# Kernel optimization log

Measured on AMD Instinct MI355X. Metric: run time of the kernel, lower is better.

Reference implementation:

```python
import jax, jax.numpy as jnp
import numpy as np

SAMPLE_RATE = 32000.0
NUM_APPLICATIONS = 3


def _eq_biquad(x, freq, gain, q, sr):
    """torchaudio.functional.equalizer_biquad: peaking EQ biquad + lfilter.
    x: [B, T] float; freq/gain/q: scalars.
    """
    w0 = 2.0 * jnp.pi * freq / sr
    A = jnp.exp(gain / 40.0 * jnp.log(10.0))  # 10 ** (gain / 40)
    alpha = jnp.sin(w0) / (2.0 * q)
    b0 = 1.0 + alpha * A
    b1 = -2.0 * jnp.cos(w0)
    b2 = 1.0 - alpha * A
    a0 = 1.0 + alpha / A
    a1 = -2.0 * jnp.cos(w0)
    a2 = 1.0 - alpha / A
    # normalize by a0 (as torchaudio biquad -> lfilter does)
    b0, b1, b2 = b0 / a0, b1 / a0, b2 / a0
    a1, a2 = a1 / a0, a2 / a0

    B = x.shape[0]
    z = jnp.zeros((B,), x.dtype)

    def step(carry, xn):
        x1, x2, y1, y2 = carry
        yn = b0 * xn + b1 * x1 + b2 * x2 - a1 * y1 - a2 * y2
        return (xn, x1, yn, y1), yn

    # scan over time axis; carry is per-batch state vectors
    _, y = jax.lax.scan(step, (z, z, z, z), x.T)  # y: [T, B]
    return y.T


def setup_inputs() -> dict:
    key = jax.random.key(0)
    k1, k2, k3, k4 = jax.random.split(key, 4)
    clip = jax.random.normal(k1, (128, 160000), dtype=jnp.float32)
    # draws within the module's f/g/q ranges
    freqs = jax.random.uniform(k2, (NUM_APPLICATIONS,), jnp.float32, 100.0, 6000.0)
    gains = jax.random.uniform(k3, (NUM_APPLICATIONS,), jnp.float32, -8.0, 8.0)
    qs = jax.random.uniform(k4, (NUM_APPLICATIONS,), jnp.float32, 1.0, 9.0)
    return {"clip": clip, "freqs": freqs, "gains": gains, "qs": qs}


def reference(clip, freqs, gains, qs):
    x = clip
    for i in range(NUM_APPLICATIONS):
        x = _eq_biquad(x, freqs[i], gains[i], qs[i], SAMPLE_RATE)
    return x
```

## Files before the change

kernel.cpp:

```cpp
#include <hip/hip_runtime.h>
#include <math.h>

#define SRATE 32000.f
#define NB 128
#define NT 160000
#define CL 100
#define NCROW 1600
#define SEG 25
#define RECROW (NCROW*8)
#define NCHUNK (NB*NCROW)
#define NBLK (NCHUNK/64)

#ifndef M_PI
#define M_PI 3.14159265358979323846
#endif

__device__ __forceinline__ void coeffs_f32(
    const float* fr, const float* gn, const float* qs, float* c)
{
  #pragma unroll
  for (int f = 0; f < 3; ++f) {
    float w0 = 2.f * (float)M_PI * fr[f] / SRATE;
    float A  = expf(gn[f] * (2.302585093f / 40.f));
    float al = sinf(w0) / (2.f * qs[f]);
    float cw = cosf(w0);
    float a0 = 1.f + al / A;
    c[f*5+0] = (1.f + al*A) / a0;
    c[f*5+1] = -2.f * cw / a0;
    c[f*5+2] = (1.f - al*A) / a0;
    c[f*5+3] = -2.f * cw / a0;
    c[f*5+4] = (1.f - al/A) / a0;
  }
}

#define STEPR(xn, res) do { \
    float y1 = c[0]*(xn) + c[1]*x1  + c[2]*x2   - c[3]*y1p  - c[4]*y1pp;  \
    float y2 = c[5]*y1  + c[6]*y1p + c[7]*y1pp - c[8]*y2p  - c[9]*y2pp;   \
    float y3 = c[10]*y2 + c[11]*y2p + c[12]*y2pp - c[13]*y3p - c[14]*y3pp;\
    (res) = y3;                                                            \
    x2 = x1; x1 = (xn);                                                    \
    y1pp=y1p; y1p=y1; y2pp=y2p; y2p=y2; y3pp=y3p; y3p=y3;                  \
  } while (0)

#define LDG5(S, base) \
  S##0 = xp[(base)];   S##1 = xp[(base)+1]; S##2 = xp[(base)+2]; \
  S##3 = xp[(base)+3]; S##4 = xp[(base)+4];

#define PRC4(v) do { float d_; STEPR(v.x, d_); (void)d_; STEPR(v.y, d_); \
                     STEPR(v.z, d_); STEPR(v.w, d_); } while (0)
#define PRC5(S) PRC4(S##0); PRC4(S##1); PRC4(S##2); PRC4(S##3); PRC4(S##4);

__global__ __launch_bounds__(64) void eq_a(
    const float* __restrict__ x, const float* __restrict__ fr,
    const float* __restrict__ gn, const float* __restrict__ qs,
    float* __restrict__ eoT)
{
  const int gch = blockIdx.x * 64 + threadIdx.x;
  const int row = gch / NCROW, ci = gch % NCROW;
  float c[15];
  coeffs_f32(fr, gn, qs, c);
  const float4* xp = (const float4*)(x + (size_t)gch * CL);
  float x1 = 0.f, x2 = 0.f;
  if (ci != 0) {
    float2 h = *(const float2*)(x + (size_t)gch * CL - 2);
    x1 = h.y; x2 = h.x;
  }
  float y1p=0,y1pp=0,y2p=0,y2pp=0,y3p=0,y3pp=0;
  float4 A0,A1,A2,A3,A4, B0,B1,B2,B3,B4;
  LDG5(A, 0);
  LDG5(B, 5);   PRC5(A);
  LDG5(A, 10);  PRC5(B);
  LDG5(B, 15);  PRC5(A);
  LDG5(A, 20);  PRC5(B);
  PRC5(A);
  const int plane = ci % SEG, slot = ci / SEG;
  float* ep = eoT + (size_t)row * RECROW + ((size_t)(plane*64 + slot))*8;
  float4 r0; r0.x=y1p; r0.y=y1pp; r0.z=y2p; r0.w=y2pp;
  float4 r1; r1.x=y3p; r1.y=y3pp; r1.z=0.f; r1.w=0.f;
  *(float4*)ep = r0; *(float4*)(ep+4) = r1;
}

__global__ __launch_bounds__(64) void eq_b(
    const float* __restrict__ fr, const float* __restrict__ gn,
    const float* __restrict__ qs, const float* __restrict__ eoT,
    float* __restrict__ sgD)
{
  __shared__ double Mb[36], Rb[36], Tb[36];
  __shared__ float Hs[36], Gs[6*36];
  const int l = threadIdx.x, row = blockIdx.x;
  float c[15];
  coeffs_f32(fr, gn, qs, c);
  if (l < 6) {
    double s0=0,s1=0,s2=0,s3=0,s4=0,s5=0;
    if (l==0) s0=1; else if (l==1) s1=1; else if (l==2) s2=1;
    else if (l==3) s3=1; else if (l==4) s4=1; else s5=1;
    double y1 = -(double)c[3]*s0 - (double)c[4]*s1;
    double y2 = (double)c[5]*y1 + (double)c[6]*s0 + (double)c[7]*s1
              - (double)c[8]*s2 - (double)c[9]*s3;
    double y3 = (double)c[10]*y2 + (double)c[11]*s2 + (double)c[12]*s3
              - (double)c[13]*s4 - (double)c[14]*s5;
    Mb[0*6+l]=y1; Mb[1*6+l]=s0; Mb[2*6+l]=y2; Mb[3*6+l]=s2; Mb[4*6+l]=y3; Mb[5*6+l]=s4;
  }
  if (l < 36) Rb[l] = ((l % 7) == 0) ? 1.0 : 0.0;
  __syncthreads();
  const int i = l / 6, j = l % 6;
  int e = CL;
  while (e) {
    if (e & 1) {
      double acc = 0.0;
      if (l < 36) { for (int k = 0; k < 6; ++k) acc += Rb[i*6+k]*Mb[k*6+j]; Tb[l]=acc; }
      __syncthreads();
      if (l < 36) Rb[l] = Tb[l];
      __syncthreads();
    }
    e >>= 1;
    if (e) {
      double acc = 0.0;
      if (l < 36) { for (int k = 0; k < 6; ++k) acc += Mb[i*6+k]*Mb[k*6+j]; Tb[l]=acc; }
      __syncthreads();
      if (l < 36) Mb[l] = Tb[l];
      __syncthreads();
    }
  }
  if (l < 36) { Hs[l] = (float)Rb[l]; Mb[l] = Rb[l]; }
  __syncthreads();
  if (l < 36) Rb[l] = ((l % 7) == 0) ? 1.0 : 0.0;
  __syncthreads();
  e = SEG;
  while (e) {
    if (e & 1) {
      double acc = 0.0;
      if (l < 36) { for (int k = 0; k < 6; ++k) acc += Rb[i*6+k]*Mb[k*6+j]; Tb[l]=acc; }
      __syncthreads();
      if (l < 36) Rb[l] = Tb[l];
      __syncthreads();
    }
    e >>= 1;
    if (e) {
      double acc = 0.0;
      if (l < 36) { for (int k = 0; k < 6; ++k) acc += Mb[i*6+k]*Mb[k*6+j]; Tb[l]=acc; }
      __syncthreads();
      if (l < 36) Mb[l] = Tb[l];
      __syncthreads();
    }
  }
  if (l < 36) Gs[l] = (float)Rb[l];
  __syncthreads();
  for (int k = 1; k < 6; ++k) {
    double acc = 0.0;
    if (l < 36) { for (int m = 0; m < 6; ++m) acc += Rb[i*6+m]*Rb[m*6+j]; Tb[l]=acc; }
    __syncthreads();
    if (l < 36) Rb[l] = Tb[l];
    __syncthreads();
    if (l < 36) Gs[k*36+l] = (float)Rb[l];
    __syncthreads();
  }

  float H[36];
  #pragma unroll
  for (int q = 0; q < 36; ++q) H[q] = Hs[q];
  const float* rbase = eoT + (size_t)row * RECROW;
  float u[6] = {0,0,0,0,0,0};
  for (int jj = 0; jj < SEG; ++jj) {
    const float* ep = rbase + ((size_t)jj*64 + l)*8;
    float4 r0 = *(const float4*)ep, r1 = *(const float4*)(ep+4);
    float ev[6] = {r0.x,r0.y,r0.z,r0.w,r1.x,r1.y};
    float nu[6];
    #pragma unroll
    for (int q = 0; q < 6; ++q) {
      float a = ev[q];
      #pragma unroll
      for (int m = 0; m < 6; ++m) a += H[q*6+m]*u[m];
      nu[q] = a;
    }
    #pragma unroll
    for (int q = 0; q < 6; ++q) u[q] = nu[q];
  }
  float v6[6];
  #pragma unroll
  for (int q = 0; q < 6; ++q) v6[q] = u[q];
  #pragma unroll
  for (int k = 0; k < 6; ++k) {
    const float* G = Gs + k*36;
    float o[6];
    #pragma unroll
    for (int q = 0; q < 6; ++q) o[q] = __shfl_up(v6[q], 1u << k, 64);
    if (l >= (1 << k)) {
      float nv[6];
      #pragma unroll
      for (int q = 0; q < 6; ++q) {
        float a = v6[q];
        #pragma unroll
        for (int m = 0; m < 6; ++m) a += G[q*6+m]*o[m];
        nv[q] = a;
      }
      #pragma unroll
      for (int q = 0; q < 6; ++q) v6[q] = nv[q];
    }
  }
  float s[6];
  #pragma unroll
  for (int q = 0; q < 6; ++q) s[q] = __shfl_up(v6[q], 1, 64);
  if (l == 0) {
    #pragma unroll
    for (int q = 0; q < 6; ++q) s[q] = 0.f;
  }
  float* wbase = sgD + (size_t)row * RECROW;
  for (int jj = 0; jj < SEG; ++jj) {
    const float* ep = rbase + ((size_t)jj*64 + l)*8;
    float4 r0 = *(const float4*)ep, r1 = *(const float4*)(ep+4);
    float ev[6] = {r0.x,r0.y,r0.z,r0.w,r1.x,r1.y};
    float* wp = wbase + ((size_t)l*SEG + jj)*8;
    float4 w0; w0.x=s[0]; w0.y=s[1]; w0.z=s[2]; w0.w=s[3];
    float4 w1; w1.x=s[4]; w1.y=s[5]; w1.z=0.f; w1.w=0.f;
    *(float4*)wp = w0; *(float4*)(wp+4) = w1;
    float ns[6];
    #pragma unroll
    for (int q = 0; q < 6; ++q) {
      float a = ev[q];
      #pragma unroll
      for (int m = 0; m < 6; ++m) a += H[q*6+m]*s[m];
      ns[q] = a;
    }
    #pragma unroll
    for (int q = 0; q < 6; ++q) s[q] = ns[q];
  }
}

__global__ __launch_bounds__(64) void eq_c(
    const float* __restrict__ x, const float* __restrict__ fr,
    const float* __restrict__ gn, const float* __restrict__ qs,
    const float* __restrict__ sgD, float* __restrict__ y)
{
  __shared__ float lds[64 * CL];
  const int j = threadIdx.x;
  const int t = blockIdx.x;
  const int gch = t * 64 + j;
  const int row = gch / NCROW, ci = gch % NCROW;
  float c[15];
  coeffs_f32(fr, gn, qs, c);
  const float* xg = x + (size_t)t * (64 * CL);
  #pragma unroll
  for (int it = 0; it < 25; ++it) {
    const int f = it * 64 + j;
    float4 v = *(const float4*)(xg + 4*f);
    *(float4*)(&lds[4*f]) = v;
  }
  __syncthreads();
  float x1, x2;
  if (j == 0) {
    if (ci == 0) { x1 = 0.f; x2 = 0.f; }
    else { float2 h = *(const float2*)(xg - 2); x1 = h.y; x2 = h.x; }
  } else {
    x1 = lds[(j-1)*CL + 99];
    x2 = lds[(j-1)*CL + 98];
  }
  const float* sp = sgD + (size_t)row * RECROW + (size_t)ci * 8;
  float4 s0 = *(const float4*)sp, s1 = *(const float4*)(sp+4);
  float y1p=s0.x, y1pp=s0.y, y2p=s0.z, y2pp=s0.w, y3p=s1.x, y3pp=s1.y;
  float* myrow = &lds[j * CL];
  #pragma unroll
  for (int k = 0; k < 25; ++k) {
    float4 xv = *(const float4*)(myrow + 4*k);
    float4 o_;
    STEPR(xv.x, o_.x); STEPR(xv.y, o_.y);
    STEPR(xv.z, o_.z); STEPR(xv.w, o_.w);
    *(float4*)(myrow + 4*k) = o_;
  }
  __syncthreads();
  float* yg = y + (size_t)t * (64 * CL);
  #pragma unroll
  for (int it = 0; it < 25; ++it) {
    const int f = it * 64 + j;
    float4 v = *(const float4*)(&lds[4*f]);
    *(float4*)(yg + 4*f) = v;
  }
}

extern "C" void kernel_launch(void* const* d_in, const int* in_sizes, int n_in,
                              void* d_out, int out_size, void* d_ws, size_t ws_size,
                              hipStream_t stream) {
  const float* clip = (const float*)d_in[0];
  const float* fr   = (const float*)d_in[1];
  const float* gn   = (const float*)d_in[2];
  const float* qs   = (const float*)d_in[3];
  float* out = (float*)d_out;
  float* eoT = (float*)d_ws;
  float* sgD = eoT + (size_t)NB * RECROW;

  eq_a<<<NBLK, 64, 0, stream>>>(clip, fr, gn, qs, eoT);
  eq_b<<<NB, 64, 0, stream>>>(fr, gn, qs, eoT, sgD);
  eq_c<<<NBLK, 64, 0, stream>>>(clip, fr, gn, qs, sgD, out);
}
```

Measured before the change: 75.52 us.

## Halve chunk length, use 128-thread blocks with async global-to-LDS staging

```diff
diff --git a/kernel.cpp b/kernel.cpp
--- a/kernel.cpp
+++ b/kernel.cpp
@@ -4,12 +4,14 @@
 #define SRATE 32000.f
 #define NB 128
 #define NT 160000
-#define CL 100
-#define NCROW 1600
-#define SEG 25
+#define CL 50
+#define TPB 128
+#define NCROW 3200
+#define BPR 25
+#define NBLK (NB*BPR)
+#define SEG 50
+#define TILEF (TPB*CL)
 #define RECROW (NCROW*8)
-#define NCHUNK (NB*NCROW)
-#define NBLK (NCHUNK/64)
 
 #ifndef M_PI
 #define M_PI 3.14159265358979323846
@@ -42,39 +44,52 @@
     y1pp=y1p; y1p=y1; y2pp=y2p; y2p=y2; y3pp=y3p; y3p=y3;                  \
   } while (0)
 
-#define LDG5(S, base) \
-  S##0 = xp[(base)];   S##1 = xp[(base)+1]; S##2 = xp[(base)+2]; \
-  S##3 = xp[(base)+3]; S##4 = xp[(base)+4];
-
-#define PRC4(v) do { float d_; STEPR(v.x, d_); (void)d_; STEPR(v.y, d_); \
-                     STEPR(v.z, d_); STEPR(v.w, d_); } while (0)
-#define PRC5(S) PRC4(S##0); PRC4(S##1); PRC4(S##2); PRC4(S##3); PRC4(S##4);
-
-__global__ __launch_bounds__(64) void eq_a(
+__device__ __forceinline__ void stage_half(
+    const float* __restrict__ src0, float* dst0, int lane)
+{
+  const float* src = src0 + lane * 4;
+  #pragma unroll
+  for (int cc = 0; cc < 12; ++cc) {
+    __builtin_amdgcn_global_load_lds(
+        (const __attribute__((address_space(1))) void*)(src + cc*256),
+        (__attribute__((address_space(3))) void*)(dst0 + cc*256), 16, 0, 0);
+  }
+  if (lane < 32) {
+    __builtin_amdgcn_global_load_lds(
+        (const __attribute__((address_space(1))) void*)(src + 12*256),
+        (__attribute__((address_space(3))) void*)(dst0 + 12*256), 16, 0, 0);
+  }
+}
+
+
+__global__ __launch_bounds__(TPB) void eq_a(
     const float* __restrict__ x, const float* __restrict__ fr,
     const float* __restrict__ gn, const float* __restrict__ qs,
     float* __restrict__ eoT)
 {
-  const int gch = blockIdx.x * 64 + threadIdx.x;
-  const int row = gch / NCROW, ci = gch % NCROW;
+  __shared__ float lds[TILEF];
+  const int tid = threadIdx.x, lane = tid & 63, w = tid >> 6;
+  const int t = blockIdx.x, row = t / BPR, bi = t % BPR;
   float c[15];
   coeffs_f32(fr, gn, qs, c);
-  const float4* xp = (const float4*)(x + (size_t)gch * CL);
-  float x1 = 0.f, x2 = 0.f;
-  if (ci != 0) {
-    float2 h = *(const float2*)(x + (size_t)gch * CL - 2);
-    x1 = h.y; x2 = h.x;
-  }
+  const float* base = x + (size_t)row * NT + bi * TILEF;
+  stage_half(base + w*3200, &lds[w*3200], lane);
+  __syncthreads();
+  const int ci = bi * TPB + tid;
+  float bx1, bx2;
+  if (tid == 0) {
+    if (bi == 0) { bx1 = 0.f; bx2 = 0.f; }
+    else { bx1 = base[-1]; bx2 = base[-2]; }
+  } else {
+    bx1 = lds[tid*CL - 1]; bx2 = lds[tid*CL - 2];
+  }
+  float x1 = bx1, x2 = bx2;
   float y1p=0,y1pp=0,y2p=0,y2pp=0,y3p=0,y3pp=0;
-  float4 A0,A1,A2,A3,A4, B0,B1,B2,B3,B4;
-  LDG5(A, 0);
-  LDG5(B, 5);   PRC5(A);
-  LDG5(A, 10);  PRC5(B);
-  LDG5(B, 15);  PRC5(A);
-  LDG5(A, 20);  PRC5(B);
-  PRC5(A);
-  const int plane = ci % SEG, slot = ci / SEG;
-  float* ep = eoT + (size_t)row * RECROW + ((size_t)(plane*64 + slot))*8;
+  #pragma unroll
+  for (int k = 0; k < CL; ++k) {
+    float d_; STEPR(lds[tid*CL + k], d_); (void)d_;
+  }
+  float* ep = eoT + (size_t)row * RECROW + ((size_t)((ci%50)*64 + ci/50))*8;
   float4 r0; r0.x=y1p; r0.y=y1pp; r0.z=y2p; r0.w=y2pp;
   float4 r1; r1.x=y3p; r1.y=y3pp; r1.z=0.f; r1.w=0.f;
   *(float4*)ep = r0; *(float4*)(ep+4) = r1;
@@ -83,7 +98,7 @@
 __global__ __launch_bounds__(64) void eq_b(
     const float* __restrict__ fr, const float* __restrict__ gn,
     const float* __restrict__ qs, const float* __restrict__ eoT,
-    float* __restrict__ sgD)
+    float* __restrict__ sgT)
 {
   __shared__ double Mb[36], Rb[36], Tb[36];
   __shared__ float Hs[36], Gs[6*36];
@@ -205,12 +220,12 @@
     #pragma unroll
     for (int q = 0; q < 6; ++q) s[q] = 0.f;
   }
-  float* wbase = sgD + (size_t)row * RECROW;
+  float* wbase = sgT + (size_t)row * RECROW;
   for (int jj = 0; jj < SEG; ++jj) {
     const float* ep = rbase + ((size_t)jj*64 + l)*8;
     float4 r0 = *(const float4*)ep, r1 = *(const float4*)(ep+4);
     float ev[6] = {r0.x,r0.y,r0.z,r0.w,r1.x,r1.y};
-    float* wp = wbase + ((size_t)l*SEG + jj)*8;
+    float* wp = wbase + ((size_t)jj*64 + l)*8;
     float4 w0; w0.x=s[0]; w0.y=s[1]; w0.z=s[2]; w0.w=s[3];
     float4 w1; w1.x=s[4]; w1.y=s[5]; w1.z=0.f; w1.w=0.f;
     *(float4*)wp = w0; *(float4*)(wp+4) = w1;
@@ -227,54 +242,48 @@
   }
 }
 
-__global__ __launch_bounds__(64) void eq_c(
+__global__ __launch_bounds__(TPB) void eq_c(
     const float* __restrict__ x, const float* __restrict__ fr,
     const float* __restrict__ gn, const float* __restrict__ qs,
-    const float* __restrict__ sgD, float* __restrict__ y)
-{
-  __shared__ float lds[64 * CL];
-  const int j = threadIdx.x;
-  const int t = blockIdx.x;
-  const int gch = t * 64 + j;
-  const int row = gch / NCROW, ci = gch % NCROW;
+    const float* __restrict__ sgT, float* __restrict__ y)
+{
+  __shared__ float lds[TILEF];
+  const int tid = threadIdx.x, lane = tid & 63, w = tid >> 6;
+  const int t = blockIdx.x, row = t / BPR, bi = t % BPR;
   float c[15];
   coeffs_f32(fr, gn, qs, c);
-  const float* xg = x + (size_t)t * (64 * CL);
-  #pragma unroll
-  for (int it = 0; it < 25; ++it) {
-    const int f = it * 64 + j;
-    float4 v = *(const float4*)(xg + 4*f);
-    *(float4*)(&lds[4*f]) = v;
-  }
-  __syncthreads();
-  float x1, x2;
-  if (j == 0) {
-    if (ci == 0) { x1 = 0.f; x2 = 0.f; }
-    else { float2 h = *(const float2*)(xg - 2); x1 = h.y; x2 = h.x; }
+  const float* base = x + (size_t)row * NT + bi * TILEF;
+  stage_half(base + w*3200, &lds[w*3200], lane);
+  __syncthreads();
+  const int ci = bi * TPB + tid;
+  float bx1, bx2;
+  if (tid == 0) {
+    if (bi == 0) { bx1 = 0.f; bx2 = 0.f; }
+    else { bx1 = base[-1]; bx2 = base[-2]; }
   } else {
-    x1 = lds[(j-1)*CL + 99];
-    x2 = lds[(j-1)*CL + 98];
-  }
-  const float* sp = sgD + (size_t)row * RECROW + (size_t)ci * 8;
+    bx1 = lds[tid*CL - 1]; bx2 = lds[tid*CL - 2];
+  }
+  const float* sp = sgT + (size_t)row * RECROW
+                  + ((size_t)((ci%50)*64 + ci/50))*8;
   float4 s0 = *(const float4*)sp, s1 = *(const float4*)(sp+4);
+  __syncthreads();
+  float x1 = bx1, x2 = bx2;
   float y1p=s0.x, y1pp=s0.y, y2p=s0.z, y2pp=s0.w, y3p=s1.x, y3pp=s1.y;
-  float* myrow = &lds[j * CL];
-  #pragma unroll
-  for (int k = 0; k < 25; ++k) {
-    float4 xv = *(const float4*)(myrow + 4*k);
-    float4 o_;
-    STEPR(xv.x, o_.x); STEPR(xv.y, o_.y);
-    STEPR(xv.z, o_.z); STEPR(xv.w, o_.w);
-    *(float4*)(myrow + 4*k) = o_;
-  }
-  __syncthreads();
-  float* yg = y + (size_t)t * (64 * CL);
-  #pragma unroll
-  for (int it = 0; it < 25; ++it) {
-    const int f = it * 64 + j;
-    float4 v = *(const float4*)(&lds[4*f]);
-    *(float4*)(yg + 4*f) = v;
-  }
+  float* myrow = &lds[tid * CL];
+  #pragma unroll
+  for (int k = 0; k < CL; ++k) {
+    float o_;
+    STEPR(myrow[k], o_);
+    myrow[k] = o_;
+  }
+  __syncthreads();
+  float* yg = y + (size_t)row * NT + bi * TILEF;
+  const float4* l4 = (const float4*)lds;
+  float4* yg4 = (float4*)yg;
+  #pragma unroll
+  for (int it = 0; it < 12; ++it)
+    yg4[it*TPB + tid] = l4[it*TPB + tid];
+  if (tid < 64) yg4[1536 + tid] = l4[1536 + tid];
 }
 
 extern "C" void kernel_launch(void* const* d_in, const int* in_sizes, int n_in,
@@ -286,9 +295,9 @@
   const float* qs   = (const float*)d_in[3];
   float* out = (float*)d_out;
   float* eoT = (float*)d_ws;
-  float* sgD = eoT + (size_t)NB * RECROW;
-
-  eq_a<<<NBLK, 64, 0, stream>>>(clip, fr, gn, qs, eoT);
-  eq_b<<<NB, 64, 0, stream>>>(fr, gn, qs, eoT, sgD);
-  eq_c<<<NBLK, 64, 0, stream>>>(clip, fr, gn, qs, sgD, out);
-}
+  float* sgT = eoT + (size_t)NB * RECROW;
+
+  eq_a<<<NBLK, TPB, 0, stream>>>(clip, fr, gn, qs, eoT);
+  eq_b<<<NB, 64, 0, stream>>>(fr, gn, qs, eoT, sgT);
+  eq_c<<<NBLK, TPB, 0, stream>>>(clip, fr, gn, qs, sgT, out);
+}
```

Result: slower. 80.25 us (+6.3%).

## Fuse chunk-state and row-scan kernels via last-block-done atomic counter

Applied to the files above, without the earlier changes.

```diff
diff --git a/kernel.cpp b/kernel.cpp
--- a/kernel.cpp
+++ b/kernel.cpp
@@ -7,6 +7,7 @@
 #define CL 100
 #define NCROW 1600
 #define SEG 25
+#define BPR 25
 #define RECROW (NCROW*8)
 #define NCHUNK (NB*NCROW)
 #define NBLK (NCHUNK/64)
@@ -50,46 +51,51 @@
                      STEPR(v.z, d_); STEPR(v.w, d_); } while (0)
 #define PRC5(S) PRC4(S##0); PRC4(S##1); PRC4(S##2); PRC4(S##3); PRC4(S##4);
 
-__global__ __launch_bounds__(64) void eq_a(
+__global__ __launch_bounds__(64) void eq_ab(
     const float* __restrict__ x, const float* __restrict__ fr,
     const float* __restrict__ gn, const float* __restrict__ qs,
-    float* __restrict__ eoT)
+    float* __restrict__ eoT, float* __restrict__ sgD,
+    int* __restrict__ cnt)
 {
-  const int gch = blockIdx.x * 64 + threadIdx.x;
+  const int tid = threadIdx.x;
+  const int gch = blockIdx.x * 64 + tid;
   const int row = gch / NCROW, ci = gch % NCROW;
   float c[15];
   coeffs_f32(fr, gn, qs, c);
-  const float4* xp = (const float4*)(x + (size_t)gch * CL);
-  float x1 = 0.f, x2 = 0.f;
-  if (ci != 0) {
-    float2 h = *(const float2*)(x + (size_t)gch * CL - 2);
-    x1 = h.y; x2 = h.x;
-  }
-  float y1p=0,y1pp=0,y2p=0,y2pp=0,y3p=0,y3pp=0;
-  float4 A0,A1,A2,A3,A4, B0,B1,B2,B3,B4;
-  LDG5(A, 0);
-  LDG5(B, 5);   PRC5(A);
-  LDG5(A, 10);  PRC5(B);
-  LDG5(B, 15);  PRC5(A);
-  LDG5(A, 20);  PRC5(B);
-  PRC5(A);
-  const int plane = ci % SEG, slot = ci / SEG;
-  float* ep = eoT + (size_t)row * RECROW + ((size_t)(plane*64 + slot))*8;
-  float4 r0; r0.x=y1p; r0.y=y1pp; r0.z=y2p; r0.w=y2pp;
-  float4 r1; r1.x=y3p; r1.y=y3pp; r1.z=0.f; r1.w=0.f;
-  *(float4*)ep = r0; *(float4*)(ep+4) = r1;
-}
-
-__global__ __launch_bounds__(64) void eq_b(
-    const float* __restrict__ fr, const float* __restrict__ gn,
-    const float* __restrict__ qs, const float* __restrict__ eoT,
-    float* __restrict__ sgD)
-{
+  {
+    const float4* xp = (const float4*)(x + (size_t)gch * CL);
+    float x1 = 0.f, x2 = 0.f;
+    if (ci != 0) {
+      float2 h = *(const float2*)(x + (size_t)gch * CL - 2);
+      x1 = h.y; x2 = h.x;
+    }
+    float y1p=0,y1pp=0,y2p=0,y2pp=0,y3p=0,y3pp=0;
+    float4 A0,A1,A2,A3,A4, B0,B1,B2,B3,B4;
+    LDG5(A, 0);
+    LDG5(B, 5);   PRC5(A);
+    LDG5(A, 10);  PRC5(B);
+    LDG5(B, 15);  PRC5(A);
+    LDG5(A, 20);  PRC5(B);
+    PRC5(A);
+    const int plane = ci % SEG, slot = ci / SEG;
+    float* ep = eoT + (size_t)row * RECROW + ((size_t)(plane*64 + slot))*8;
+    float4 r0; r0.x=y1p; r0.y=y1pp; r0.z=y2p; r0.w=y2pp;
+    float4 r1; r1.x=y3p; r1.y=y3pp; r1.z=0.f; r1.w=0.f;
+    *(float4*)ep = r0; *(float4*)(ep+4) = r1;
+  }
+
+  __threadfence();
+  __shared__ int s_old;
+  if (tid == 0)
+    s_old = __hip_atomic_fetch_add(&cnt[row], 1, __ATOMIC_ACQ_REL,
+                                   __HIP_MEMORY_SCOPE_AGENT);
+  __syncthreads();
+  if (s_old != BPR - 1) return;
+  __threadfence();
+
   __shared__ double Mb[36], Rb[36], Tb[36];
   __shared__ float Hs[36], Gs[6*36];
-  const int l = threadIdx.x, row = blockIdx.x;
-  float c[15];
-  coeffs_f32(fr, gn, qs, c);
+  const int l = tid;
   if (l < 6) {
     double s0=0,s1=0,s2=0,s3=0,s4=0,s5=0;
     if (l==0) s0=1; else if (l==1) s1=1; else if (l==2) s2=1;
@@ -240,6 +246,8 @@
   float c[15];
   coeffs_f32(fr, gn, qs, c);
   const float* xg = x + (size_t)t * (64 * CL);
+  const float* sp = sgD + (size_t)row * RECROW + (size_t)ci * 8;
+  float4 s0 = *(const float4*)sp, s1 = *(const float4*)(sp+4);
   #pragma unroll
   for (int it = 0; it < 25; ++it) {
     const int f = it * 64 + j;
@@ -255,8 +263,6 @@
     x1 = lds[(j-1)*CL + 99];
     x2 = lds[(j-1)*CL + 98];
   }
-  const float* sp = sgD + (size_t)row * RECROW + (size_t)ci * 8;
-  float4 s0 = *(const float4*)sp, s1 = *(const float4*)(sp+4);
   float y1p=s0.x, y1pp=s0.y, y2p=s0.z, y2pp=s0.w, y3p=s1.x, y3pp=s1.y;
   float* myrow = &lds[j * CL];
   #pragma unroll
@@ -287,8 +293,9 @@
   float* out = (float*)d_out;
   float* eoT = (float*)d_ws;
   float* sgD = eoT + (size_t)NB * RECROW;
-
-  eq_a<<<NBLK, 64, 0, stream>>>(clip, fr, gn, qs, eoT);
-  eq_b<<<NB, 64, 0, stream>>>(fr, gn, qs, eoT, sgD);
+  int*   cnt = (int*)(sgD + (size_t)NB * RECROW);
+
+  hipMemsetAsync(cnt, 0, NB * sizeof(int), stream);
+  eq_ab<<<NBLK, 64, 0, stream>>>(clip, fr, gn, qs, eoT, sgD, cnt);
   eq_c<<<NBLK, 64, 0, stream>>>(clip, fr, gn, qs, sgD, out);
 }
```

Result: slower. 298.4 us (+295.1%).

## Write zero-state outputs in pass one and apply linear state correction afterwards

Applied to the files above, without the earlier changes.

```diff
diff --git a/kernel.cpp b/kernel.cpp
--- a/kernel.cpp
+++ b/kernel.cpp
@@ -10,6 +10,7 @@
 #define RECROW (NCROW*8)
 #define NCHUNK (NB*NCROW)
 #define NBLK (NCHUNK/64)
+#define WPAD 104
 
 #ifndef M_PI
 #define M_PI 3.14159265358979323846
@@ -42,50 +43,67 @@
     y1pp=y1p; y1p=y1; y2pp=y2p; y2p=y2; y3pp=y3p; y3p=y3;                  \
   } while (0)
 
-#define LDG5(S, base) \
-  S##0 = xp[(base)];   S##1 = xp[(base)+1]; S##2 = xp[(base)+2]; \
-  S##3 = xp[(base)+3]; S##4 = xp[(base)+4];
-
-#define PRC4(v) do { float d_; STEPR(v.x, d_); (void)d_; STEPR(v.y, d_); \
-                     STEPR(v.z, d_); STEPR(v.w, d_); } while (0)
-#define PRC5(S) PRC4(S##0); PRC4(S##1); PRC4(S##2); PRC4(S##3); PRC4(S##4);
-
 __global__ __launch_bounds__(64) void eq_a(
     const float* __restrict__ x, const float* __restrict__ fr,
     const float* __restrict__ gn, const float* __restrict__ qs,
-    float* __restrict__ eoT)
+    float* __restrict__ eoT, float* __restrict__ out)
 {
-  const int gch = blockIdx.x * 64 + threadIdx.x;
+  __shared__ float lds[64 * CL];
+  const int j = threadIdx.x;
+  const int t = blockIdx.x;
+  const int gch = t * 64 + j;
   const int row = gch / NCROW, ci = gch % NCROW;
   float c[15];
   coeffs_f32(fr, gn, qs, c);
-  const float4* xp = (const float4*)(x + (size_t)gch * CL);
-  float x1 = 0.f, x2 = 0.f;
-  if (ci != 0) {
-    float2 h = *(const float2*)(x + (size_t)gch * CL - 2);
-    x1 = h.y; x2 = h.x;
+  const float* xg = x + (size_t)t * (64 * CL);
+  #pragma unroll
+  for (int it = 0; it < 25; ++it) {
+    const int f = it * 64 + j;
+    float4 v = *(const float4*)(xg + 4*f);
+    *(float4*)(&lds[4*f]) = v;
+  }
+  __syncthreads();
+  float x1, x2;
+  if (j == 0) {
+    if (ci == 0) { x1 = 0.f; x2 = 0.f; }
+    else { float2 h = *(const float2*)(xg - 2); x1 = h.y; x2 = h.x; }
+  } else {
+    x1 = lds[(j-1)*CL + 99];
+    x2 = lds[(j-1)*CL + 98];
   }
   float y1p=0,y1pp=0,y2p=0,y2pp=0,y3p=0,y3pp=0;
-  float4 A0,A1,A2,A3,A4, B0,B1,B2,B3,B4;
-  LDG5(A, 0);
-  LDG5(B, 5);   PRC5(A);
-  LDG5(A, 10);  PRC5(B);
-  LDG5(B, 15);  PRC5(A);
-  LDG5(A, 20);  PRC5(B);
-  PRC5(A);
-  const int plane = ci % SEG, slot = ci / SEG;
-  float* ep = eoT + (size_t)row * RECROW + ((size_t)(plane*64 + slot))*8;
-  float4 r0; r0.x=y1p; r0.y=y1pp; r0.z=y2p; r0.w=y2pp;
-  float4 r1; r1.x=y3p; r1.y=y3pp; r1.z=0.f; r1.w=0.f;
-  *(float4*)ep = r0; *(float4*)(ep+4) = r1;
+  float* myrow = &lds[j * CL];
+  #pragma unroll
+  for (int k = 0; k < 25; ++k) {
+    float4 xv = *(const float4*)(myrow + 4*k);
+    float4 o_;
+    STEPR(xv.x, o_.x); STEPR(xv.y, o_.y);
+    STEPR(xv.z, o_.z); STEPR(xv.w, o_.w);
+    *(float4*)(myrow + 4*k) = o_;
+  }
+  {
+    const int plane = ci % SEG, slot = ci / SEG;
+    float* ep = eoT + (size_t)row * RECROW + ((size_t)(plane*64 + slot))*8;
+    float4 r0; r0.x=y1p; r0.y=y1pp; r0.z=y2p; r0.w=y2pp;
+    float4 r1; r1.x=y3p; r1.y=y3pp; r1.z=0.f; r1.w=0.f;
+    *(float4*)ep = r0; *(float4*)(ep+4) = r1;
+  }
+  __syncthreads();
+  float* yg = out + (size_t)t * (64 * CL);
+  #pragma unroll
+  for (int it = 0; it < 25; ++it) {
+    const int f = it * 64 + j;
+    float4 v = *(const float4*)(&lds[4*f]);
+    *(float4*)(yg + 4*f) = v;
+  }
 }
 
 __global__ __launch_bounds__(64) void eq_b(
     const float* __restrict__ fr, const float* __restrict__ gn,
     const float* __restrict__ qs, const float* __restrict__ eoT,
-    float* __restrict__ sgD)
+    float* __restrict__ sgD, float* __restrict__ Wg)
 {
-  __shared__ double Mb[36], Rb[36], Tb[36];
+  __shared__ double Mb[36], Rb[36], Tb[36], Mk[36], wv[8], wn[8];
   __shared__ float Hs[36], Gs[6*36];
   const int l = threadIdx.x, row = blockIdx.x;
   float c[15];
@@ -103,6 +121,8 @@
   }
   if (l < 36) Rb[l] = ((l % 7) == 0) ? 1.0 : 0.0;
   __syncthreads();
+  if (l < 36) Mk[l] = Mb[l];
+  __syncthreads();
   const int i = l / 6, j = l % 6;
   int e = CL;
   while (e) {
@@ -154,6 +174,18 @@
     __syncthreads();
     if (l < 36) Gs[k*36+l] = (float)Rb[l];
     __syncthreads();
+  }
+  if (row == 0) {
+    if (l < 6) wv[l] = (l == 4) ? 1.0 : 0.0;
+    __syncthreads();
+    for (int k = 0; k < CL; ++k) {
+      if (l < 6) { double a = 0.0;
+        for (int m = 0; m < 6; ++m) a += wv[m]*Mk[m*6+l];
+        wn[l] = a; }
+      __syncthreads();
+      if (l < 6) { wv[l] = wn[l]; Wg[l*WPAD + k] = (float)wn[l]; }
+      __syncthreads();
+    }
   }
 
   float H[36];
@@ -227,53 +259,33 @@
   }
 }
 
-__global__ __launch_bounds__(64) void eq_c(
-    const float* __restrict__ x, const float* __restrict__ fr,
-    const float* __restrict__ gn, const float* __restrict__ qs,
-    const float* __restrict__ sgD, float* __restrict__ y)
+__global__ __launch_bounds__(256) void eq_corr(
+    float* __restrict__ out, const float* __restrict__ sgD,
+    const float* __restrict__ Wg)
 {
-  __shared__ float lds[64 * CL];
-  const int j = threadIdx.x;
-  const int t = blockIdx.x;
-  const int gch = t * 64 + j;
-  const int row = gch / NCROW, ci = gch % NCROW;
-  float c[15];
-  coeffs_f32(fr, gn, qs, c);
-  const float* xg = x + (size_t)t * (64 * CL);
-  #pragma unroll
-  for (int it = 0; it < 25; ++it) {
-    const int f = it * 64 + j;
-    float4 v = *(const float4*)(xg + 4*f);
-    *(float4*)(&lds[4*f]) = v;
-  }
-  __syncthreads();
-  float x1, x2;
-  if (j == 0) {
-    if (ci == 0) { x1 = 0.f; x2 = 0.f; }
-    else { float2 h = *(const float2*)(xg - 2); x1 = h.y; x2 = h.x; }
-  } else {
-    x1 = lds[(j-1)*CL + 99];
-    x2 = lds[(j-1)*CL + 98];
-  }
-  const float* sp = sgD + (size_t)row * RECROW + (size_t)ci * 8;
-  float4 s0 = *(const float4*)sp, s1 = *(const float4*)(sp+4);
-  float y1p=s0.x, y1pp=s0.y, y2p=s0.z, y2pp=s0.w, y3p=s1.x, y3pp=s1.y;
-  float* myrow = &lds[j * CL];
-  #pragma unroll
-  for (int k = 0; k < 25; ++k) {
-    float4 xv = *(const float4*)(myrow + 4*k);
-    float4 o_;
-    STEPR(xv.x, o_.x); STEPR(xv.y, o_.y);
-    STEPR(xv.z, o_.z); STEPR(xv.w, o_.w);
-    *(float4*)(myrow + 4*k) = o_;
-  }
-  __syncthreads();
-  float* yg = y + (size_t)t * (64 * CL);
-  #pragma unroll
-  for (int it = 0; it < 25; ++it) {
-    const int f = it * 64 + j;
-    float4 v = *(const float4*)(&lds[4*f]);
-    *(float4*)(yg + 4*f) = v;
+  __shared__ float Wl[6*WPAD];
+  const int tid = threadIdx.x;
+  for (int i = tid; i < 6*WPAD; i += 256) Wl[i] = Wg[i];
+  __syncthreads();
+  const size_t total = (size_t)NCHUNK * 25;
+  float4* o4 = (float4*)out;
+  for (size_t f = (size_t)blockIdx.x*256 + tid; f < total;
+       f += (size_t)gridDim.x*256) {
+    const size_t cch = f / 25;
+    const int kq = (int)(f % 25);
+    const float* sp = sgD + cch*8;
+    float4 s0 = *(const float4*)sp, s1 = *(const float4*)(sp+4);
+    const float sg[6] = {s0.x,s0.y,s0.z,s0.w,s1.x,s1.y};
+    float4 yv = o4[f];
+    #pragma unroll
+    for (int j = 0; j < 6; ++j) {
+      float4 w4 = *(const float4*)(&Wl[j*WPAD + kq*4]);
+      yv.x += w4.x * sg[j];
+      yv.y += w4.y * sg[j];
+      yv.z += w4.z * sg[j];
+      yv.w += w4.w * sg[j];
+    }
+    o4[f] = yv;
   }
 }
 
@@ -287,8 +299,9 @@
   float* out = (float*)d_out;
   float* eoT = (float*)d_ws;
   float* sgD = eoT + (size_t)NB * RECROW;
-
-  eq_a<<<NBLK, 64, 0, stream>>>(clip, fr, gn, qs, eoT);
-  eq_b<<<NB, 64, 0, stream>>>(fr, gn, qs, eoT, sgD);
-  eq_c<<<NBLK, 64, 0, stream>>>(clip, fr, gn, qs, sgD, out);
-}
+  float* Wg  = sgD + (size_t)NB * RECROW;
+
+  eq_a<<<NBLK, 64, 0, stream>>>(clip, fr, gn, qs, eoT, out);
+  eq_b<<<NB, 64, 0, stream>>>(fr, gn, qs, eoT, sgD, Wg);
+  eq_corr<<<2048, 256, 0, stream>>>(out, sgD, Wg);
+}
```

Result: slower. 94.43 us (+25.0%).
